# Performance work log

Hardware: AMD Instinct MI355X
Metric: run time of the kernel (lower is better)

## Reference

```python
import jax, jax.numpy as jnp
import numpy as np

D_MODEL = 1024
N_HEAD = 16
D_HEAD = D_MODEL // N_HEAD


def setup_inputs() -> dict:
    key = jax.random.key(0)
    ks = jax.random.split(key, 12)
    L, B, M = 2048, 2, 2048
    s = 1.0 / np.sqrt(D_MODEL)
    return {
        "q": jax.random.normal(ks[0], (L, B, D_MODEL), jnp.float32),
        "kv": jax.random.normal(ks[1], (L, B, D_MODEL), jnp.float32),
        "mem": jax.random.normal(ks[2], (M, B, D_MODEL), jnp.float32),
        "w_q": jax.random.normal(ks[3], (D_MODEL, D_MODEL), jnp.float32) * s,
        "b_q": jnp.zeros((D_MODEL,), jnp.float32),
        "w_k": jax.random.normal(ks[4], (D_MODEL, D_MODEL), jnp.float32) * s,
        "b_k": jnp.zeros((D_MODEL,), jnp.float32),
        "w_v": jax.random.normal(ks[5], (D_MODEL, D_MODEL), jnp.float32) * s,
        "b_v": jnp.zeros((D_MODEL,), jnp.float32),
        "w_c": jax.random.normal(ks[6], (D_MODEL, D_MODEL), jnp.float32) * s,
        "b_c": jnp.zeros((D_MODEL,), jnp.float32),
    }


def reference(q, kv, mem, w_q, b_q, w_k, b_k, w_v, b_v, w_c, b_c):
    # c: [L+M, B, D]
    c = jnp.concatenate([mem, kv], axis=0)
    L, B, _ = q.shape
    J = c.shape[0]
    # linear projections (torch Linear: x @ W^T + b)
    qh = (q @ w_q.T + b_q).reshape(L, B, N_HEAD, D_HEAD)
    kh = (c @ w_k.T + b_k).reshape(J, B, N_HEAD, D_HEAD)
    vh = (c @ w_v.T + b_v).reshape(J, B, N_HEAD, D_HEAD)
    # attention scores [i, j, b, n]
    score = jnp.einsum("ibnd,jbnd->ijbn", qh, kh) / np.sqrt(D_HEAD).astype(np.float32)
    prob = jax.nn.softmax(score, axis=1)
    vec = jnp.einsum("ijbn,jbnd->ibnd", prob, vh).reshape(L, B, D_MODEL)
    return vec @ w_c.T + b_c
```

## Files before the change

### kernel.cpp

```cpp
#include <hip/hip_runtime.h>


using short8 = __attribute__((ext_vector_type(8))) short;
using f32x4  = __attribute__((ext_vector_type(4))) float;

#define DEV __device__ __forceinline__

DEV unsigned short f2bf(float f) {
  union { float f; unsigned int u; } x; x.f = f;
  unsigned int r = x.u + 0x7FFFu + ((x.u >> 16) & 1u);
  return (unsigned short)(r >> 16);
}

DEV unsigned int cvtpk(float lo, float hi) {
  unsigned int r;
  asm("v_cvt_pk_bf16_f32 %0, %1, %2" : "=v"(r) : "v"(lo), "v"(hi));
  return r;
}

DEV void gload_lds16(const unsigned short* g, unsigned short* l) {
  __builtin_amdgcn_global_load_lds(
      (const __attribute__((address_space(1))) unsigned int*)g,
      (__attribute__((address_space(3))) unsigned int*)l, 16, 0, 0);
}

__global__ __launch_bounds__(256) void convert_all(
    const float* __restrict__ q, const float* __restrict__ mem_,
    const float* __restrict__ kv, const float* __restrict__ wq,
    const float* __restrict__ wk, const float* __restrict__ wv,
    const float* __restrict__ wc, unsigned short* __restrict__ a_bf,
    unsigned short* __restrict__ c_bf, unsigned short* __restrict__ w_bf) {
  size_t u = (size_t)blockIdx.x * 256 + threadIdx.x;
  const float* src;
  unsigned short* dst;
  if (u < 524288u)        { src = q    + u * 8;                dst = a_bf + u * 8; }
  else if (u < 1048576u)  { src = mem_ + (u - 524288u) * 8;    dst = c_bf + (u - 524288u) * 8; }
  else if (u < 1572864u)  { src = kv   + (u - 1048576u) * 8;   dst = c_bf + 4194304u + (u - 1048576u) * 8; }
  else if (u < 1703936u)  { src = wq   + (u - 1572864u) * 8;   dst = w_bf + (u - 1572864u) * 8; }
  else if (u < 1835008u)  { src = wk   + (u - 1703936u) * 8;   dst = w_bf + 1048576u + (u - 1703936u) * 8; }
  else if (u < 1966080u)  { src = wv   + (u - 1835008u) * 8;   dst = w_bf + 2097152u + (u - 1835008u) * 8; }
  else                    { src = wc   + (u - 1966080u) * 8;   dst = w_bf + 3145728u + (u - 1966080u) * 8; }
  float4 v0 = ((const float4*)src)[0];
  float4 v1 = ((const float4*)src)[1];
  union { unsigned short us[8]; uint4 v; } o;
  o.us[0] = f2bf(v0.x); o.us[1] = f2bf(v0.y); o.us[2] = f2bf(v0.z); o.us[3] = f2bf(v0.w);
  o.us[4] = f2bf(v1.x); o.us[5] = f2bf(v1.y); o.us[6] = f2bf(v1.z); o.us[7] = f2bf(v1.w);
  *(uint4*)dst = o.v;
}

template <int MODE>
__global__ __launch_bounds__(256, 2) void gemm_bt(
    const unsigned short* __restrict__ A, const unsigned short* __restrict__ Bw,
    const float* __restrict__ bias, void* __restrict__ outp) {
  __shared__ __align__(16) unsigned short lA[128 * 64];
  __shared__ __align__(16) unsigned short lB[128 * 64];
  const int tid = threadIdx.x;
  const int lane = tid & 63;
  const int w = tid >> 6;
  const int wr = w >> 1, wcn = w & 1;
  const int tm = blockIdx.x * 128;
  const int tn = blockIdx.y * 128;

  const int srow = lane >> 3;
  const int scol = ((lane & 7) ^ srow) * 8;
  const unsigned short* aptr = A + (size_t)(tm + 32 * w + srow) * 1024 + scol;
  const unsigned short* bptr = Bw + (size_t)(tn + 32 * w + srow) * 1024 + scol;
  unsigned short* lAw = &lA[(32 * w) * 64];
  unsigned short* lBw = &lB[(32 * w) * 64];

  const f32x4 zero = {0.f, 0.f, 0.f, 0.f};
  f32x4 acc[4][4];
#pragma unroll
  for (int i = 0; i < 4; ++i)
#pragma unroll
    for (int j = 0; j < 4; ++j) acc[i][j] = zero;

  for (int kb = 0; kb < 16; ++kb) {
    const int ko = kb * 64;
#pragma unroll
    for (int c = 0; c < 4; ++c) {
      gload_lds16(aptr + ko + c * 8 * 1024, lAw + c * 8 * 64);
      gload_lds16(bptr + ko + c * 8 * 1024, lBw + c * 8 * 64);
    }
    __syncthreads();
#pragma unroll
    for (int kk = 0; kk < 2; ++kk) {
      short8 af[4], bfr[4];
#pragma unroll
      for (int mi = 0; mi < 4; ++mi) {
        int r = 64 * wr + 16 * mi + (lane & 15);
        int slot = (kk * 4 + (lane >> 4)) ^ (r & 7);
        af[mi] = *(const short8*)&lA[r * 64 + slot * 8];
      }
#pragma unroll
      for (int ni = 0; ni < 4; ++ni) {
        int r = 64 * wcn + 16 * ni + (lane & 15);
        int slot = (kk * 4 + (lane >> 4)) ^ (r & 7);
        bfr[ni] = *(const short8*)&lB[r * 64 + slot * 8];
      }
#pragma unroll
      for (int mi = 0; mi < 4; ++mi)
#pragma unroll
        for (int ni = 0; ni < 4; ++ni)
          acc[mi][ni] = __builtin_amdgcn_mfma_f32_16x16x32_bf16(
              af[mi], bfr[ni], acc[mi][ni], 0, 0, 0);
    }
    __syncthreads();
  }

  const int g4 = (lane >> 4) * 4;
  const int c0 = lane & 15;
#pragma unroll
  for (int mi = 0; mi < 4; ++mi) {
#pragma unroll
    for (int ni = 0; ni < 4; ++ni) {
      const int colt = tn + 64 * wcn + 16 * ni + c0;
      const float bv = bias[colt];
#pragma unroll
      for (int j = 0; j < 4; ++j) {
        const int rowt = tm + 64 * wr + 16 * mi + g4 + j;
        const float v = acc[mi][ni][j] + bv;
        if constexpr (MODE == 0) {
          ((float*)outp)[(size_t)rowt * 1024 + colt] = v;
        } else if constexpr (MODE == 1) {
          const int i = rowt >> 1, b = rowt & 1, n = colt >> 6, d = colt & 63;
          ((unsigned short*)outp)[(((size_t)(b * 16 + n) * 2048 + i) << 6) + d] =
              f2bf(v * 0.1803368801111f);
        } else if constexpr (MODE == 2) {
          const int jj = rowt >> 1, b = rowt & 1, n = colt >> 6, d = colt & 63;
          ((unsigned short*)outp)[(((size_t)(b * 16 + n) * 4096 + jj) << 6) + d] = f2bf(v);
        } else {
          const int jj = rowt >> 1, b = rowt & 1, n = colt >> 6, d = colt & 63;
          const int j6 = jj & 63;
          const int pos = (j6 & 3) | (((j6 >> 4) & 1) << 2) | (((j6 >> 2) & 3) << 3) |
                          (((j6 >> 5) & 1) << 5);
          ((unsigned short*)outp)[((size_t)(b * 16 + n) * 64 + d) * 4096 + (jj & ~63) + pos] =
              f2bf(v);
        }
      }
    }
  }
}

__global__ __launch_bounds__(256, 4) void attn_kernel(
    const unsigned short* __restrict__ qh, const unsigned short* __restrict__ kh,
    const unsigned short* __restrict__ vt, unsigned short* __restrict__ vec) {
  __shared__ __align__(16) unsigned short kl[2][64 * 64];
  __shared__ __align__(16) unsigned short vl[2][64 * 64];
  const int tid = threadIdx.x;
  const int lane = tid & 63;
  const int w = tid >> 6;
  const int g = lane >> 4;
  const int l4 = lane & 15;
  const int f = blockIdx.x;
  const int qt = (f >> 3) & 31;
  const int head = (f & 7) * 4 + (f >> 8);
  const int b = head >> 4, n = head & 15;
  const unsigned short* qbase = qh + ((size_t)head * 2048 + qt * 64 + 16 * w) * 64;
  const unsigned short* kbase = kh + (size_t)head * 4096 * 64;
  const unsigned short* vbase = vt + (size_t)head * 64 * 4096;

  short8 qf[2];
#pragma unroll
  for (int kk = 0; kk < 2; ++kk)
    qf[kk] = *(const short8*)&qbase[l4 * 64 + kk * 32 + g * 8];

  const f32x4 zero = {0.f, 0.f, 0.f, 0.f};
  f32x4 oacc[4];
#pragma unroll
  for (int nd = 0; nd < 4; ++nd) oacc[nd] = zero;
  float mrow = -3.0e38f;
  float lrow = 0.f;

  const int srow = lane >> 3;
  const int scol = ((lane & 7) ^ srow) * 8;
  const unsigned short* kp0 = kbase + (size_t)(16 * w + srow) * 64 + scol;
  const unsigned short* kp1 = kbase + (size_t)(16 * w + 8 + srow) * 64 + scol;
  const unsigned short* vp0 = vbase + (size_t)(16 * w + srow) * 4096 + scol;
  const unsigned short* vp1 = vbase + (size_t)(16 * w + 8 + srow) * 4096 + scol;

  auto stage = [&](int jt, int bufi) {
    gload_lds16(kp0 + (size_t)jt * 4096, &kl[bufi][(16 * w) * 64]);
    gload_lds16(kp1 + (size_t)jt * 4096, &kl[bufi][(16 * w + 8) * 64]);
    gload_lds16(vp0 + jt * 64, &vl[bufi][(16 * w) * 64]);
    gload_lds16(vp1 + jt * 64, &vl[bufi][(16 * w + 8) * 64]);
  };

  stage(0, 0);
  __syncthreads();

  for (int jt = 0; jt < 64; ++jt) {
    const int buf = jt & 1;
    if (jt < 63) stage(jt + 1, buf ^ 1);

    f32x4 s[4];
#pragma unroll
    for (int nj = 0; nj < 4; ++nj) s[nj] = zero;
#pragma unroll
    for (int kk = 0; kk < 2; ++kk) {
      short8 bk[4];
#pragma unroll
      for (int nj = 0; nj < 4; ++nj) {
        int r = 16 * nj + l4;
        int slot = (kk * 4 + g) ^ (r & 7);
        bk[nj] = *(const short8*)&kl[buf][r * 64 + slot * 8];
      }
#pragma unroll
      for (int nj = 0; nj < 4; ++nj)
        s[nj] = __builtin_amdgcn_mfma_f32_16x16x32_bf16(bk[nj], qf[kk], s[nj], 0, 0, 0);
    }

    {
      float a0 = fmaxf(fmaxf(s[0][0], s[0][1]), fmaxf(s[0][2], s[0][3]));
      float a1 = fmaxf(fmaxf(s[1][0], s[1][1]), fmaxf(s[1][2], s[1][3]));
      float a2 = fmaxf(fmaxf(s[2][0], s[2][1]), fmaxf(s[2][2], s[2][3]));
      float a3 = fmaxf(fmaxf(s[3][0], s[3][1]), fmaxf(s[3][2], s[3][3]));
      float pmax = fmaxf(fmaxf(a0, a1), fmaxf(a2, a3));
      pmax = fmaxf(pmax, __shfl_xor(pmax, 16));
      pmax = fmaxf(pmax, __shfl_xor(pmax, 32));
      if (!__all(pmax <= mrow + 8.f)) {
        const float mnew = fmaxf(mrow, pmax);
        const float sc = __builtin_amdgcn_exp2f(mrow - mnew);
        mrow = mnew;
        lrow *= sc;
#pragma unroll
        for (int reg = 0; reg < 4; ++reg) {
          const float scr = __shfl(sc, 4 * g + reg);
#pragma unroll
          for (int nd = 0; nd < 4; ++nd) oacc[nd][reg] *= scr;
        }
      }
      const float m = mrow;
      float rs = 0.f;
#pragma unroll
      for (int nj = 0; nj < 4; ++nj)
#pragma unroll
        for (int reg = 0; reg < 4; ++reg) {
          const float p = __builtin_amdgcn_exp2f(s[nj][reg] - m);
          s[nj][reg] = p;
          rs += p;
        }
      rs += __shfl_xor(rs, 16);
      rs += __shfl_xor(rs, 32);
      lrow += rs;
    }

    short8 pa[2];
#pragma unroll
    for (int kk2 = 0; kk2 < 2; ++kk2) {
      union { unsigned int u[4]; short8 v; } t;
#pragma unroll
      for (int wd = 0; wd < 4; ++wd) {
        const int nj = (wd >> 1) + 2 * kk2;
        const int r0 = (wd & 1) * 2;
        t.u[wd] = cvtpk(s[nj][r0], s[nj][r0 + 1]);
      }
      pa[kk2] = t.v;
    }

#pragma unroll
    for (int kk2 = 0; kk2 < 2; ++kk2) {
      short8 bv4[4];
#pragma unroll
      for (int nd = 0; nd < 4; ++nd) {
        const int r = 16 * nd + l4;
        const int blk = (g + 4 * kk2) ^ (r & 7);
        bv4[nd] = *(const short8*)&vl[buf][r * 64 + blk * 8];
      }
#pragma unroll
      for (int nd = 0; nd < 4; ++nd)
        oacc[nd] = __builtin_amdgcn_mfma_f32_16x16x32_bf16(pa[kk2], bv4[nd], oacc[nd], 0, 0, 0);
    }
    __syncthreads();
  }

#pragma unroll
  for (int reg = 0; reg < 4; ++reg) {
    const float lr = __shfl(lrow, 4 * g + reg);
    const float inv = 1.f / lr;
    const int i = qt * 64 + 16 * w + 4 * g + reg;
#pragma unroll
    for (int nd = 0; nd < 4; ++nd) {
      const int d = 16 * nd + l4;
      vec[(size_t)(i * 2 + b) * 1024 + n * 64 + d] = f2bf(oacc[nd][reg] * inv);
    }
  }
}

extern "C" void kernel_launch(void* const* d_in, const int* in_sizes, int n_in,
                              void* d_out, int out_size, void* d_ws, size_t ws_size,
                              hipStream_t stream) {
  (void)in_sizes; (void)n_in; (void)out_size; (void)ws_size;
  const float* q    = (const float*)d_in[0];
  const float* kv   = (const float*)d_in[1];
  const float* mem_ = (const float*)d_in[2];
  const float* wq   = (const float*)d_in[3];
  const float* bq   = (const float*)d_in[4];
  const float* wk   = (const float*)d_in[5];
  const float* bk   = (const float*)d_in[6];
  const float* wv   = (const float*)d_in[7];
  const float* bv   = (const float*)d_in[8];
  const float* wc   = (const float*)d_in[9];
  const float* bc   = (const float*)d_in[10];

  char* ws = (char*)d_ws;
  unsigned short* w_bf = (unsigned short*)(ws);
  unsigned short* a_bf = (unsigned short*)(ws + (8ull << 20));
  unsigned short* c_bf = (unsigned short*)(ws + (16ull << 20));
  unsigned short* qhb  = (unsigned short*)(ws + (32ull << 20));
  unsigned short* khb  = (unsigned short*)(ws + (40ull << 20));
  unsigned short* vtb  = (unsigned short*)(ws + (56ull << 20));
  unsigned short* vecb = a_bf;

  convert_all<<<8192, 256, 0, stream>>>(q, mem_, kv, wq, wk, wv, wc, a_bf, c_bf, w_bf);
  gemm_bt<1><<<dim3(32, 8), 256, 0, stream>>>(a_bf, w_bf,                bq, qhb);
  gemm_bt<2><<<dim3(64, 8), 256, 0, stream>>>(c_bf, w_bf + (1u << 20),   bk, khb);
  gemm_bt<3><<<dim3(64, 8), 256, 0, stream>>>(c_bf, w_bf + (2u << 20),   bv, vtb);
  attn_kernel<<<1024, 256, 0, stream>>>(qhb, khb, vtb, vecb);
  gemm_bt<0><<<dim3(32, 8), 256, 0, stream>>>(vecb, w_bf + (3u << 20),   bc, d_out);
}
```

Measured before the change: 210.3 us.

## Enlarge attention blocks to 128 queries with triple-buffered K/V staging

The attention kernel now runs 512 threads (8 waves) per block, covering 128 query rows, so each K/V tile staged in shared memory is reused by twice as many waves and half the global K/V traffic is issued per query. Staging moves to a three-deep ring with prefetch distance two, explicit vmcnt waits and raw barriers in place of __syncthreads, so loads overlap with more compute. The grid halves to 512 blocks, which may reduce occupancy balance across CUs, and the hand-written waitcnt logic must stay exact or the kernel reads stale tiles.

```diff
diff --git a/kernel.cpp b/kernel.cpp
--- a/kernel.cpp
+++ b/kernel.cpp
@@ -23,6 +23,13 @@
       (const __attribute__((address_space(1))) unsigned int*)g,
       (__attribute__((address_space(3))) unsigned int*)l, 16, 0, 0);
 }
+
+#define BARRIER_RAW()                      \
+  do {                                     \
+    __builtin_amdgcn_sched_barrier(0);     \
+    __builtin_amdgcn_s_barrier();          \
+    __builtin_amdgcn_sched_barrier(0);     \
+  } while (0)
 
 __global__ __launch_bounds__(256) void convert_all(
     const float* __restrict__ q, const float* __restrict__ mem_,
@@ -142,21 +149,21 @@
   }
 }
 
-__global__ __launch_bounds__(256, 4) void attn_kernel(
+__global__ __launch_bounds__(512, 4) void attn_kernel(
     const unsigned short* __restrict__ qh, const unsigned short* __restrict__ kh,
     const unsigned short* __restrict__ vt, unsigned short* __restrict__ vec) {
-  __shared__ __align__(16) unsigned short kl[2][64 * 64];
-  __shared__ __align__(16) unsigned short vl[2][64 * 64];
+  __shared__ __align__(16) unsigned short kl[3][64 * 64];
+  __shared__ __align__(16) unsigned short vl[3][64 * 64];
   const int tid = threadIdx.x;
   const int lane = tid & 63;
   const int w = tid >> 6;
   const int g = lane >> 4;
   const int l4 = lane & 15;
   const int f = blockIdx.x;
-  const int qt = (f >> 3) & 31;
-  const int head = (f & 7) * 4 + (f >> 8);
+  const int head = (f & 7) * 4 + ((f >> 3) & 3);
+  const int qt = f >> 5;
   const int b = head >> 4, n = head & 15;
-  const unsigned short* qbase = qh + ((size_t)head * 2048 + qt * 64 + 16 * w) * 64;
+  const unsigned short* qbase = qh + ((size_t)head * 2048 + qt * 128 + 16 * w) * 64;
   const unsigned short* kbase = kh + (size_t)head * 4096 * 64;
   const unsigned short* vbase = vt + (size_t)head * 64 * 4096;
 
@@ -174,24 +181,22 @@
 
   const int srow = lane >> 3;
   const int scol = ((lane & 7) ^ srow) * 8;
-  const unsigned short* kp0 = kbase + (size_t)(16 * w + srow) * 64 + scol;
-  const unsigned short* kp1 = kbase + (size_t)(16 * w + 8 + srow) * 64 + scol;
-  const unsigned short* vp0 = vbase + (size_t)(16 * w + srow) * 4096 + scol;
-  const unsigned short* vp1 = vbase + (size_t)(16 * w + 8 + srow) * 4096 + scol;
+  const unsigned short* kp = kbase + (size_t)(8 * w + srow) * 64 + scol;
+  const unsigned short* vp = vbase + (size_t)(8 * w + srow) * 4096 + scol;
 
   auto stage = [&](int jt, int bufi) {
-    gload_lds16(kp0 + (size_t)jt * 4096, &kl[bufi][(16 * w) * 64]);
-    gload_lds16(kp1 + (size_t)jt * 4096, &kl[bufi][(16 * w + 8) * 64]);
-    gload_lds16(vp0 + jt * 64, &vl[bufi][(16 * w) * 64]);
-    gload_lds16(vp1 + jt * 64, &vl[bufi][(16 * w + 8) * 64]);
+    gload_lds16(kp + (size_t)jt * 4096, &kl[bufi][(8 * w) * 64]);
+    gload_lds16(vp + jt * 64, &vl[bufi][(8 * w) * 64]);
   };
 
   stage(0, 0);
-  __syncthreads();
+  stage(1, 1);
+  asm volatile("s_waitcnt vmcnt(2)" ::: "memory");
+  BARRIER_RAW();
 
   for (int jt = 0; jt < 64; ++jt) {
-    const int buf = jt & 1;
-    if (jt < 63) stage(jt + 1, buf ^ 1);
+    const int buf = jt % 3;
+    if (jt + 2 < 64) stage(jt + 2, (jt + 2) % 3);
 
     f32x4 s[4];
 #pragma unroll
@@ -271,14 +276,22 @@
       for (int nd = 0; nd < 4; ++nd)
         oacc[nd] = __builtin_amdgcn_mfma_f32_16x16x32_bf16(pa[kk2], bv4[nd], oacc[nd], 0, 0, 0);
     }
-    __syncthreads();
+
+    if (jt < 63) {
+      if (jt < 62) {
+        asm volatile("s_waitcnt vmcnt(2)" ::: "memory");
+      } else {
+        asm volatile("s_waitcnt vmcnt(0)" ::: "memory");
+      }
+      BARRIER_RAW();
+    }
   }
 
 #pragma unroll
   for (int reg = 0; reg < 4; ++reg) {
     const float lr = __shfl(lrow, 4 * g + reg);
     const float inv = 1.f / lr;
-    const int i = qt * 64 + 16 * w + 4 * g + reg;
+    const int i = qt * 128 + 16 * w + 4 * g + reg;
 #pragma unroll
     for (int nd = 0; nd < 4; ++nd) {
       const int d = 16 * nd + l4;
@@ -316,6 +329,6 @@
   gemm_bt<1><<<dim3(32, 8), 256, 0, stream>>>(a_bf, w_bf,                bq, qhb);
   gemm_bt<2><<<dim3(64, 8), 256, 0, stream>>>(c_bf, w_bf + (1u << 20),   bk, khb);
   gemm_bt<3><<<dim3(64, 8), 256, 0, stream>>>(c_bf, w_bf + (2u << 20),   bv, vtb);
-  attn_kernel<<<1024, 256, 0, stream>>>(qhb, khb, vtb, vecb);
+  attn_kernel<<<512, 512, 0, stream>>>(qhb, khb, vtb, vecb);
   gemm_bt<0><<<dim3(32, 8), 256, 0, stream>>>(vecb, w_bf + (3u << 20),   bc, d_out);
 }
```

Result: faster. 198.7 us (-5.5%).
